# Optimization experiments

Hardware: AMD Instinct MI355X
Metric: run time of the kernel (lower is better)

Reference implementation:

```python
import jax, jax.numpy as jnp
import numpy as np

# dims (see shape_source)
BS, CIN, HF, WF = 4, 256, 56, 120   # packed batch, state channels, feature HxW (image/8)
CF, D = 64, 48                      # lifted feature channels, depth bins
DOWNSAMPLE = 8                      # image->feature stride (frustum in image pixels)
BEVX = BEVY = 128                   # BEV.SIZE // BEV.FEATURE_DOWNSAMPLE
SCALE = 0.6                         # BEV.RESOLUTION * BEV.FEATURE_DOWNSAMPLE (m/cell)
OFFX = 32.0                         # BEV.OFFSET_FORWARD / BEV.FEATURE_DOWNSAMPLE
D0, DSTEP = 2.0, 1.0                # dbound = [2.0, 50.0, 1.0]


def _conv(x, w, b, pad):
    y = jax.lax.conv_general_dilated(x, w, (1, 1), [(pad, pad), (pad, pad)],
                                     dimension_numbers=('NCHW', 'OIHW', 'NCHW'))
    return y + b[None, :, None, None]


def _block(x, w, b, g, bt, pad):
    # Conv2dBlock: conv -> BN (inference, running_mean=0 / running_var=1) -> relu
    y = _conv(x, w, b, pad)
    return jax.nn.relu(g[None, :, None, None] * y + bt[None, :, None, None])


def _forward(state, intr, extr, feat_w, feat_b, feat_g, feat_bt,
             dec_w, dec_b, dec_g, dec_bt, depth_w, depth_b):
    # image feature + depth distribution heads
    x = _block(state, feat_w, feat_b, feat_g, feat_bt, 2)           # [BS,CF,HF,WF]
    df = _block(state, dec_w, dec_b, dec_g, dec_bt, 2)              # [BS,CF,HF,WF]
    depth = jax.nn.softmax(_conv(df, depth_w, depth_b, 0), axis=1)  # [BS,D,HF,WF]

    # lift: outer product of depth distribution with features
    lift = depth[:, None, :, :, :] * x[:, :, None, :, :]            # [BS,CF,D,HF,WF]
    feats = lift.transpose(0, 2, 3, 4, 1)                           # [BS,D,HF,WF,CF]

    # frustum geometry: pixel (u,v,d) -> camera -> ego frame
    ds = D0 + jnp.arange(D, dtype=jnp.float32) * DSTEP              # [D]
    u = (jnp.arange(WF, dtype=jnp.float32) + 0.5) * DOWNSAMPLE      # image-pixel u
    v = (jnp.arange(HF, dtype=jnp.float32) + 0.5) * DOWNSAMPLE      # image-pixel v
    ud = u[None, None, :] * ds[:, None, None]                       # [D,1,WF] bcast
    vd = v[None, :, None] * ds[:, None, None]
    dd = jnp.broadcast_to(ds[:, None, None], (D, HF, WF))
    pix = jnp.stack(jnp.broadcast_arrays(ud, vd, dd), axis=-1)      # [D,HF,WF,3]
    Kinv = jnp.linalg.inv(intr)
    cam = pix @ Kinv.T                                              # camera frame
    R, t = extr[:3, :3], extr[:3, 3]
    ego = cam @ R.T + t                                             # [D,HF,WF,3]

    # voxelize into BEV grid + scatter-accumulate (splat)
    ix = jnp.floor(ego[..., 0] / SCALE + OFFX + BEVX / 2).astype(jnp.int32)
    iy = jnp.floor(ego[..., 1] / SCALE + BEVY / 2).astype(jnp.int32)
    valid = (ix >= 0) & (ix < BEVX) & (iy >= 0) & (iy < BEVY)       # [D,HF,WF]
    cell = iy * BEVX + ix
    batch_off = (jnp.arange(BS, dtype=jnp.int32) * (BEVY * BEVX))[:, None, None, None]
    seg = jnp.where(valid[None], batch_off + cell[None], BS * BEVY * BEVX)  # dump bin
    pooled = jax.ops.segment_sum(feats.reshape(BS * D * HF * WF, CF),
                                 seg.reshape(-1),
                                 num_segments=BS * BEVY * BEVX + 1)[:-1]
    bev = pooled.reshape(BS, BEVY, BEVX, CF).transpose(0, 3, 1, 2)  # [BS,CF,Y,X]
    return bev


def setup_inputs() -> dict:
    key = jax.random.key(0)
    ks = jax.random.split(key, 4)
    s = 0.02
    state = jax.random.normal(ks[0], (BS, CIN, HF, WF), jnp.float32)
    intr = jnp.array([[500., 0., 480.], [0., 500., 224.], [0., 0., 1.]], jnp.float32)
    # camera z -> ego x (forward), mounted at x=1.5m, z=2.0m
    extr = jnp.array([[0., 0., 1., 1.5], [-1., 0., 0., 0.],
                      [0., -1., 0., 2.0], [0., 0., 0., 1.]], jnp.float32)
    return {
        'state': state, 'intr': intr, 'extr': extr,
        'feat_w': jax.random.normal(ks[1], (CF, CIN, 5, 5), jnp.float32) * s,
        'feat_b': jnp.zeros((CF,), jnp.float32),
        'feat_g': jnp.ones((CF,), jnp.float32),
        'feat_bt': jnp.zeros((CF,), jnp.float32),
        'dec_w': jax.random.normal(ks[2], (CF, CIN, 5, 5), jnp.float32) * s,
        'dec_b': jnp.zeros((CF,), jnp.float32),
        'dec_g': jnp.ones((CF,), jnp.float32),
        'dec_bt': jnp.zeros((CF,), jnp.float32),
        'depth_w': jax.random.normal(ks[3], (D, CF, 1, 1), jnp.float32) * s,
        'depth_b': jnp.zeros((D,), jnp.float32),
    }


def reference(state, intr, extr, feat_w, feat_b, feat_g, feat_bt,
              dec_w, dec_b, dec_g, dec_bt, depth_w, depth_b):
    return _forward(state, intr, extr, feat_w, feat_b, feat_g, feat_bt,
                    dec_w, dec_b, dec_g, dec_bt, depth_w, depth_b)
```

## Files before the change

kernel.cpp:

```cpp
#include <hip/hip_runtime.h>
#include <hip/hip_bf16.h>
#include <math.h>

#define BS 4
#define CIN 256
#define HF 56
#define WF 120
#define CF 64
#define DD 48
#define HW (HF*WF)
#define BEVX 128
#define BEVY 128
#define NCELL (BEVX*BEVY)
#define NPTS (DD*HW)

#define PH 60
#define PW 124

#define PACKW_BLOCKS 400
#define CELL_BLOCKS  23

typedef short s16x8 __attribute__((ext_vector_type(8)));
typedef float f32x4 __attribute__((ext_vector_type(4)));

__device__ __forceinline__ unsigned short f2bf(float f) {
    unsigned int u = __float_as_uint(f);
    unsigned int r = (u + 0x7FFFu + ((u >> 16) & 1u)) >> 16;
    return (unsigned short)r;
}
__device__ __forceinline__ float bf2f(unsigned short s) {
    return __uint_as_float(((unsigned int)s) << 16);
}

__global__ __launch_bounds__(256) void pad_kernel(
    const float* __restrict__ state, unsigned short* __restrict__ P)
{
    __shared__ float lt[32 * 257];
    const int tile = blockIdx.x;
    const int b    = blockIdx.y;
    const int tid  = threadIdx.x;
    const int4 z4 = make_int4(0, 0, 0, 0);

    if (tile < 210) {
        const int hw0 = tile * 32;
        const int wl = tid & 31;
        const int cg = tid >> 5;
        const float* src = state + (size_t)(b * CIN + cg * 32) * HW + hw0 + wl;
#pragma unroll 8
        for (int k = 0; k < 32; ++k)
            lt[wl * 257 + cg * 32 + k] = src[(size_t)k * HW];
        __syncthreads();

        const int px = tid >> 3;
        const int ck = tid & 7;
        const int hw = hw0 + px;
        const int h = hw / WF, w = hw - h * WF;
        unsigned short* dst = P + (((size_t)b * PH + h + 2) * PW + (w + 2)) * CIN;
#pragma unroll
        for (int r = 0; r < 4; ++r) {
            const int c0 = r * 64 + ck * 8;
            unsigned short tmp[8];
#pragma unroll
            for (int j = 0; j < 8; ++j) tmp[j] = f2bf(lt[px * 257 + c0 + j]);
            *(int4*)(dst + c0) = *(const int4*)tmp;
        }
    } else {
        const int pxid = (tile - 210) * 32 + (tid >> 3);
        const int ck = tid & 7;
        if (pxid < 720) {
            int h2, w2;
            if (pxid < 496) { int r = pxid / 124; h2 = (r < 2) ? r : 56 + r; w2 = pxid - r * 124; }
            else { int u = pxid - 496; h2 = 2 + (u >> 2); int m = u & 3; w2 = (m < 2) ? m : 120 + m; }
            unsigned short* dst = P + (((size_t)b * PH + h2) * PW + w2) * CIN;
#pragma unroll
            for (int r = 0; r < 4; ++r)
                *(int4*)(dst + r * 64 + ck * 8) = z4;
        }
    }
}

__global__ __launch_bounds__(256) void prep_kernel(
    const float* __restrict__ intr, const float* __restrict__ extr,
    const float* __restrict__ fw, const float* __restrict__ dw,
    const float* __restrict__ fb, const float* __restrict__ fg, const float* __restrict__ fbt,
    const float* __restrict__ db, const float* __restrict__ dg, const float* __restrict__ dbt,
    const float* __restrict__ dpw,
    unsigned short* __restrict__ Wf, float2* __restrict__ aff,
    unsigned short* __restrict__ Wd, int* __restrict__ celltab)
{
    const int bid = blockIdx.x;
    const int tid = threadIdx.x;

    if (bid < PACKW_BLOCKS) {
        int t = bid * 256 + tid;
        int lane = t & 63;
        int nf = (t >> 6) & 7;
        int kc = (t >> 9) & 7;
        int p  = t >> 12;
        int n   = nf * 16 + (lane & 15);
        int ci0 = kc * 32 + (lane >> 4) * 8;
        const float* src = (n < 64) ? fw + (size_t)n * CIN * 25
                                    : dw + (size_t)(n - 64) * CIN * 25;
        unsigned short v[8];
#pragma unroll
        for (int j = 0; j < 8; ++j)
            v[j] = f2bf(src[(size_t)(ci0 + j) * 25 + p]);
        *(int4*)(Wf + (size_t)t * 8) = *(const int4*)v;
    } else if (bid == PACKW_BLOCKS) {
        if (tid < 128) {
            float g, bi, bt;
            if (tid < 64) { g = fg[tid]; bi = fb[tid]; bt = fbt[tid]; }
            else          { g = dg[tid - 64]; bi = db[tid - 64]; bt = dbt[tid - 64]; }
            aff[tid] = make_float2(g, g * bi + bt);
        }
        for (int e = tid; e < 384; e += 256) {
            int ln = e & 63;
            int s  = (e >> 6) & 1;
            int t  = e >> 7;
            unsigned short v[8];
#pragma unroll
            for (int j = 0; j < 8; ++j)
                v[j] = f2bf(dpw[(16 * t + (ln & 15)) * CF + s * 32 + (ln >> 4) * 8 + j]);
            *(int4*)(Wd + (size_t)e * 8) = *(const int4*)v;
        }
    } else {
        int pair = (bid - PACKW_BLOCKS - 1) * 256 + tid;
        if (pair >= DD * WF) return;
        int d = pair / WF;
        int w = pair - d * WF;
        int h = 0;

        float k00 = intr[0], k01 = intr[1], k02 = intr[2];
        float k11 = intr[4], k12 = intr[5];
        float k22 = intr[8];

        float A00 = __fdiv_rn(1.0f, k00);
        float A11 = __fdiv_rn(1.0f, k11);
        float A01 = __fmul_rn(__fmul_rn(k01, A00), -A11);
        float A22 = __fdiv_rn(1.0f, k22);
        float x0  = __fmul_rn(k02, A00);
        x0        = __fadd_rn(x0, __fmul_rn(k12, A01));
        float x1  = __fmul_rn(k12, A11);
        float A02 = __fmul_rn(x0, -A22);
        float A12 = __fmul_rn(x1, -A22);

        float i00 = A00, i01 = A01, i02 = A02;
        float i10 = 0.f, i11 = A11, i12 = A12;
        float i20 = 0.f, i21 = 0.f, i22 = A22;

        float u   = (w + 0.5f) * 8.0f;
        float v   = (h + 0.5f) * 8.0f;
        float dsv = 2.0f + (float)d;
        float px  = __fmul_rn(u, dsv);
        float py  = __fmul_rn(v, dsv);
        float pz  = dsv;

        float cam0 = fmaf(pz, i02, fmaf(py, i01, fmaf(px, i00, 0.0f)));
        float cam1 = fmaf(pz, i12, fmaf(py, i11, fmaf(px, i10, 0.0f)));
        float cam2 = fmaf(pz, i22, fmaf(py, i21, fmaf(px, i20, 0.0f)));

        float r00 = extr[0], r01 = extr[1], r02 = extr[2],  t0 = extr[3];
        float r10 = extr[4], r11 = extr[5], r12 = extr[6],  t1 = extr[7];

        float mm0 = fmaf(cam2, r02, fmaf(cam1, r01, fmaf(cam0, r00, 0.0f)));
        float mm1 = fmaf(cam2, r12, fmaf(cam1, r11, fmaf(cam0, r10, 0.0f)));
        float e0  = __fadd_rn(mm0, t0);
        float e1  = __fadd_rn(mm1, t1);

        float ixf = floorf(__fadd_rn(__fadd_rn(__fdiv_rn(e0, 0.6f), 32.0f), 64.0f));
        float iyf = floorf(__fadd_rn(__fdiv_rn(e1, 0.6f), 64.0f));
        int ix = (int)ixf;
        int iy = (int)iyf;

        bool valid = (ix >= 0) && (ix < BEVX) && (iy >= 0) && (iy < BEVY);
        celltab[pair] = valid ? iy * BEVX + ix : -1;
    }
}

__global__ __launch_bounds__(256) void conv_mfma_kernel(
    const unsigned short* __restrict__ P, const unsigned short* __restrict__ Wf,
    const float2* __restrict__ aff,
    unsigned short* __restrict__ xTb, unsigned short* __restrict__ decB)
{
    __shared__ __align__(16) unsigned short lds[2][144 * 32];

    const int tid  = threadIdx.x;
    const int lane = tid & 63;
    const int wid  = tid >> 6;
    const int wm   = wid >> 1;
    const int wn_g = ((blockIdx.z & 1) << 1) + (wid & 1);
    const int b  = blockIdx.z >> 1;
    const int h0 = blockIdx.y * 8;
    const int w0 = blockIdx.x * 8;

    const unsigned short* Pb = P + (((size_t)b * PH + h0) * PW + w0) * CIN;

    const int pix0 = tid >> 2,          slot0 = tid & 3;
    const size_t g0 = ((size_t)(pix0 / 12) * PW + (pix0 % 12)) * CIN + slot0 * 8;
    const int l0 = pix0 * 32 + (slot0 ^ ((pix0 >> 1) & 3)) * 8;
    const int c1 = 256 + tid;
    const int pix1 = c1 >> 2,           slot1 = c1 & 3;
    const size_t g1 = ((size_t)(pix1 / 12) * PW + (pix1 % 12)) * CIN + slot1 * 8;
    const int l1 = pix1 * 32 + (slot1 ^ ((pix1 >> 1) & 3)) * 8;
    const int c2 = 512 + tid;
    const int pix2 = c2 >> 2,           slot2 = c2 & 3;
    const size_t g2 = ((size_t)(pix2 / 12) * PW + (pix2 % 12)) * CIN + slot2 * 8;
    const int l2 = pix2 * 32 + (slot2 ^ ((pix2 >> 1) & 3)) * 8;
    const bool has3 = (tid < 64);

    f32x4 acc[2][2];
#pragma unroll
    for (int i = 0; i < 2; ++i)
#pragma unroll
        for (int j = 0; j < 2; ++j)
            acc[i][j] = (f32x4){0.f, 0.f, 0.f, 0.f};

    const int kg = lane >> 4;
    const int m0 = wm * 32 + (lane & 15);
    const int m1 = m0 + 16;
    const int pb0 = ((m0 >> 3)) * 12 + (m0 & 7);
    const int pb1 = ((m1 >> 3)) * 12 + (m1 & 7);

    {
        int4 r0 = *(const int4*)(Pb + g0);
        int4 r1 = *(const int4*)(Pb + g1);
        int4 r2;
        if (has3) r2 = *(const int4*)(Pb + g2);
        *(int4*)((char*)lds[0] + (size_t)l0 * 2) = r0;
        *(int4*)((char*)lds[0] + (size_t)l1 * 2) = r1;
        if (has3) *(int4*)((char*)lds[0] + (size_t)l2 * 2) = r2;
    }
    __syncthreads();

    for (int kc = 0; kc < 8; ++kc) {
        const int cur = kc & 1;
        int4 n0, n1, n2;
        if (kc < 7) {
            n0 = *(const int4*)(Pb + g0 + (size_t)(kc + 1) * 32);
            n1 = *(const int4*)(Pb + g1 + (size_t)(kc + 1) * 32);
            if (has3) n2 = *(const int4*)(Pb + g2 + (size_t)(kc + 1) * 32);
        }
        const unsigned short* lb = lds[cur];
#pragma unroll 5
        for (int p = 0; p < 25; ++p) {
            const int poff = (p / 5) * 12 + (p % 5);
            const int px0 = pb0 + poff;
            const int px1 = pb1 + poff;
            s16x8 a0 = *(const s16x8*)(lb + px0 * 32 + (kg ^ ((px0 >> 1) & 3)) * 8);
            s16x8 a1 = *(const s16x8*)(lb + px1 * 32 + (kg ^ ((px1 >> 1) & 3)) * 8);
            const size_t we = (((size_t)(p * 8 + kc) * 8) + wn_g * 2) * 64 + lane;
            s16x8 b0 = *(const s16x8*)(Wf + we * 8);
            s16x8 b1 = *(const s16x8*)(Wf + we * 8 + 512);
            acc[0][0] = __builtin_amdgcn_mfma_f32_16x16x32_bf16(a0, b0, acc[0][0], 0, 0, 0);
            acc[1][0] = __builtin_amdgcn_mfma_f32_16x16x32_bf16(a1, b0, acc[1][0], 0, 0, 0);
            acc[0][1] = __builtin_amdgcn_mfma_f32_16x16x32_bf16(a0, b1, acc[0][1], 0, 0, 0);
            acc[1][1] = __builtin_amdgcn_mfma_f32_16x16x32_bf16(a1, b1, acc[1][1], 0, 0, 0);
        }
        if (kc < 7) {
            *(int4*)((char*)lds[cur ^ 1] + (size_t)l0 * 2) = n0;
            *(int4*)((char*)lds[cur ^ 1] + (size_t)l1 * 2) = n1;
            if (has3) *(int4*)((char*)lds[cur ^ 1] + (size_t)l2 * 2) = n2;
        }
        __syncthreads();
    }

#pragma unroll
    for (int nf = 0; nf < 2; ++nf) {
        const int n = wn_g * 32 + nf * 16 + (lane & 15);
        const float2 sc = aff[n];
        unsigned short* dst = (n < 64) ? xTb : decB;
        const int ch = n & 63;
#pragma unroll
        for (int mf = 0; mf < 2; ++mf) {
#pragma unroll
            for (int r = 0; r < 4; ++r) {
                const int m = wm * 32 + mf * 16 + (lane >> 4) * 4 + r;
                const int h = h0 + (m >> 3), w = w0 + (m & 7);
                dst[(((size_t)b * HW) + h * WF + w) * 64 + ch] =
                    f2bf(fmaxf(sc.x * acc[mf][nf][r] + sc.y, 0.f));
            }
        }
    }
}

__global__ __launch_bounds__(256) void depth_kernel(
    const unsigned short* __restrict__ decB, const unsigned short* __restrict__ Wd,
    const float* __restrict__ dbs, float* __restrict__ depP, float4* __restrict__ poolz)
{
    {
        const int gid = blockIdx.x * 256 + threadIdx.x;
        const float4 z = make_float4(0.f, 0.f, 0.f, 0.f);
#pragma unroll
        for (int r = 0; r < 10; ++r) {
            int i = gid + r * (420 * 256);
            if (i < (BS * NCELL * CF) / 4) poolz[i] = z;
        }
    }

    const int lane = threadIdx.x & 63;
    const int wave = blockIdx.x * 4 + (threadIdx.x >> 6);
    const int px0  = wave * 16;

    const unsigned short* A = decB + (size_t)px0 * 64 + (lane & 15) * 64 + (lane >> 4) * 8;
    s16x8 a0 = *(const s16x8*)(A);
    s16x8 a1 = *(const s16x8*)(A + 32);

    f32x4 acc[3];
    float dbv[3];
#pragma unroll
    for (int t = 0; t < 3; ++t) {
        acc[t] = (f32x4){0.f, 0.f, 0.f, 0.f};
        dbv[t] = dbs[16 * t + (lane & 15)];
        s16x8 b0 = *(const s16x8*)(Wd + ((size_t)(t * 2 + 0) * 64 + lane) * 8);
        s16x8 b1 = *(const s16x8*)(Wd + ((size_t)(t * 2 + 1) * 64 + lane) * 8);
        acc[t] = __builtin_amdgcn_mfma_f32_16x16x32_bf16(a0, b0, acc[t], 0, 0, 0);
        acc[t] = __builtin_amdgcn_mfma_f32_16x16x32_bf16(a1, b1, acc[t], 0, 0, 0);
    }

#pragma unroll
    for (int r = 0; r < 4; ++r) {
        float l0 = acc[0][r] + dbv[0];
        float l1 = acc[1][r] + dbv[1];
        float l2 = acc[2][r] + dbv[2];
        float m = fmaxf(fmaxf(l0, l1), l2);
#pragma unroll
        for (int o = 1; o < 16; o <<= 1) m = fmaxf(m, __shfl_xor(m, o));
        float e0 = expf(l0 - m), e1 = expf(l1 - m), e2 = expf(l2 - m);
        float s = e0 + e1 + e2;
#pragma unroll
        for (int o = 1; o < 16; o <<= 1) s += __shfl_xor(s, o);
        float inv = 1.0f / s;
        float* op = depP + (size_t)(px0 + (lane >> 4) * 4 + r) * DD + (lane & 15);
        op[0]  = e0 * inv;
        op[16] = e1 * inv;
        op[32] = e2 * inv;
    }
}

__global__ __launch_bounds__(256) void colsum_kernel(
    const unsigned short* __restrict__ xTb, const float* __restrict__ depP,
    const int* __restrict__ celltab, float* __restrict__ pooled)
{
    const int w  = blockIdx.x;
    const int b  = blockIdx.z;
    const int lane = threadIdx.x & 63;
    const int wv   = threadIdx.x >> 6;
    const int dbase = blockIdx.y * 16 + wv * 4;

    int cells[4];
    bool anyv = false;
#pragma unroll
    for (int j = 0; j < 4; ++j) {
        cells[j] = celltab[(dbase + j) * WF + w];
        anyv |= (cells[j] >= 0);
    }
    if (!anyv) return;

    const unsigned short* xp = xTb + (((size_t)b * HW) + w) * 64 + lane;
    const float* dp = depP + (((size_t)b * HW) + w) * DD + dbase;

    float acc[4] = {0.f, 0.f, 0.f, 0.f};
#pragma unroll 8
    for (int h = 0; h < HF; ++h) {
        float xv = bf2f(xp[(size_t)h * WF * 64]);
        float4 dv = *(const float4*)(dp + (size_t)h * WF * DD);
        acc[0] = fmaf(dv.x, xv, acc[0]);
        acc[1] = fmaf(dv.y, xv, acc[1]);
        acc[2] = fmaf(dv.z, xv, acc[2]);
        acc[3] = fmaf(dv.w, xv, acc[3]);
    }

    float* pb = pooled + (size_t)b * NCELL * CF;
#pragma unroll
    for (int j = 0; j < 4; ++j)
        if (cells[j] >= 0)
            atomicAdd(&pb[(size_t)cells[j] * CF + lane], acc[j]);
}

__global__ __launch_bounds__(256) void transpose_kernel(
    const float* __restrict__ pooled, float* __restrict__ out)
{
    __shared__ float t[64][65];
    const int b  = blockIdx.y;
    const int c0 = blockIdx.x * 64;
    const int tid = threadIdx.x;
#pragma unroll
    for (int k = 0; k < 16; ++k) {
        int idx = tid + k * 256;
        int cell = idx >> 6, ch = idx & 63;
        t[cell][ch] = pooled[(((size_t)b * NCELL) + c0 + cell) * CF + ch];
    }
    __syncthreads();
#pragma unroll
    for (int k = 0; k < 16; ++k) {
        int idx = tid + k * 256;
        int ch = idx >> 6, cell = idx & 63;
        out[((size_t)b * CF + ch) * NCELL + c0 + cell] = t[cell][ch];
    }
}

extern "C" void kernel_launch(void* const* d_in, const int* in_sizes, int n_in,
                              void* d_out, int out_size, void* d_ws, size_t ws_size,
                              hipStream_t stream)
{
    const float* state   = (const float*)d_in[0];
    const float* intr    = (const float*)d_in[1];
    const float* extr    = (const float*)d_in[2];
    const float* feat_w  = (const float*)d_in[3];
    const float* feat_b  = (const float*)d_in[4];
    const float* feat_g  = (const float*)d_in[5];
    const float* feat_bt = (const float*)d_in[6];
    const float* dec_w   = (const float*)d_in[7];
    const float* dec_b   = (const float*)d_in[8];
    const float* dec_g   = (const float*)d_in[9];
    const float* dec_bt  = (const float*)d_in[10];
    const float* depth_w = (const float*)d_in[11];
    const float* depth_b = (const float*)d_in[12];
    float* out = (float*)d_out;

    char* ws = (char*)d_ws;
    const size_t P_BYTES   = (size_t)BS * PH * PW * CIN * 2;
    const size_t WF_BYTES  = (size_t)25 * 8 * 8 * 64 * 16;
    const size_t AFF_BYTES = 1024;
    const size_t WD_BYTES  = 384 * 16;
    const size_t FB_BYTES  = (size_t)BS * HW * CF * 2;
    const size_t DEP_BYTES = (size_t)BS * HW * DD * 4;
    const size_t CT_BYTES  = ((size_t)DD * WF + 64) * 4;

    unsigned short* P    = (unsigned short*)ws;           ws += P_BYTES;
    unsigned short* Wfr  = (unsigned short*)ws;           ws += WF_BYTES;
    float2*         aff  = (float2*)ws;                   ws += AFF_BYTES;
    unsigned short* Wd   = (unsigned short*)ws;           ws += WD_BYTES;
    unsigned short* xTb  = (unsigned short*)ws;           ws += FB_BYTES;
    unsigned short* decB = (unsigned short*)ws;           ws += FB_BYTES;
    float*          depP = (float*)ws;                    ws += DEP_BYTES;
    int*            celltab = (int*)ws;                   ws += CT_BYTES;

    float* pooled = (float*)d_ws;

    pad_kernel<<<dim3(233, BS), 256, 0, stream>>>(state, P);

    prep_kernel<<<PACKW_BLOCKS + 1 + CELL_BLOCKS, 256, 0, stream>>>(
        intr, extr, feat_w, dec_w,
        feat_b, feat_g, feat_bt, dec_b, dec_g, dec_bt, depth_w,
        Wfr, aff, Wd, celltab);

    conv_mfma_kernel<<<dim3(15, 7, BS * 2), 256, 0, stream>>>(
        P, Wfr, aff, xTb, decB);

    depth_kernel<<<420, 256, 0, stream>>>(decB, Wd, depth_b, depP, (float4*)pooled);

    colsum_kernel<<<dim3(WF, 3, BS), 256, 0, stream>>>(xTb, depP, celltab, pooled);

    transpose_kernel<<<dim3(NCELL / 64, BS), 256, 0, stream>>>(pooled, out);
}
```

Before: 189.7 us.

## Merge conv N-halves into one block and split taps across warp groups

The conv kernel now runs 512-thread blocks that each compute all 128 output channels (both feature and depth-decoder heads) for an 8x8 tile, instead of two blocks per tile each doing half the channels. The 25 filter taps are split between two groups of four waves, and the partial accumulators are reduced through shared memory before the epilogue. This halves redundant input-tile loads into LDS and keeps the same wave count per tile. In exchange it adds a 32KB LDS reduction buffer, an extra barrier, more accumulator registers per wave, and an uneven 13/12 tap split, which may lower occupancy.

```diff
diff --git a/kernel.cpp b/kernel.cpp
--- a/kernel.cpp
+++ b/kernel.cpp
@@ -177,19 +177,44 @@
     }
 }
 
-__global__ __launch_bounds__(256) void conv_mfma_kernel(
+#define CONV_TAPS(PL, PH_)                                                              \
+    for (int p = PL; p < PH_; ++p) {                                                    \
+        const int poff = (p / 5) * 12 + (p % 5);                                        \
+        const int px0 = pb0 + poff;                                                     \
+        const int px1 = pb1 + poff;                                                     \
+        s16x8 a0 = *(const s16x8*)(lb + px0 * 32 + (kg ^ ((px0 >> 1) & 3)) * 8);        \
+        s16x8 a1 = *(const s16x8*)(lb + px1 * 32 + (kg ^ ((px1 >> 1) & 3)) * 8);        \
+        const unsigned short* wp =                                                      \
+            Wf + ((((size_t)(p * 8 + kc)) * 8 + wn * 4) * 64 + lane) * 8;               \
+        s16x8 b0 = *(const s16x8*)(wp);                                                 \
+        s16x8 b1 = *(const s16x8*)(wp + 512);                                           \
+        s16x8 b2 = *(const s16x8*)(wp + 1024);                                          \
+        s16x8 b3 = *(const s16x8*)(wp + 1536);                                          \
+        acc[0][0] = __builtin_amdgcn_mfma_f32_16x16x32_bf16(a0, b0, acc[0][0], 0, 0, 0);\
+        acc[1][0] = __builtin_amdgcn_mfma_f32_16x16x32_bf16(a1, b0, acc[1][0], 0, 0, 0);\
+        acc[0][1] = __builtin_amdgcn_mfma_f32_16x16x32_bf16(a0, b1, acc[0][1], 0, 0, 0);\
+        acc[1][1] = __builtin_amdgcn_mfma_f32_16x16x32_bf16(a1, b1, acc[1][1], 0, 0, 0);\
+        acc[0][2] = __builtin_amdgcn_mfma_f32_16x16x32_bf16(a0, b2, acc[0][2], 0, 0, 0);\
+        acc[1][2] = __builtin_amdgcn_mfma_f32_16x16x32_bf16(a1, b2, acc[1][2], 0, 0, 0);\
+        acc[0][3] = __builtin_amdgcn_mfma_f32_16x16x32_bf16(a0, b3, acc[0][3], 0, 0, 0);\
+        acc[1][3] = __builtin_amdgcn_mfma_f32_16x16x32_bf16(a1, b3, acc[1][3], 0, 0, 0);\
+    }
+
+__global__ __launch_bounds__(512) void conv_mfma_kernel(
     const unsigned short* __restrict__ P, const unsigned short* __restrict__ Wf,
     const float2* __restrict__ aff,
     unsigned short* __restrict__ xTb, unsigned short* __restrict__ decB)
 {
     __shared__ __align__(16) unsigned short lds[2][144 * 32];
+    __shared__ __align__(16) float red[4 * 8 * 64 * 4];
 
     const int tid  = threadIdx.x;
     const int lane = tid & 63;
     const int wid  = tid >> 6;
-    const int wm   = wid >> 1;
-    const int wn_g = ((blockIdx.z & 1) << 1) + (wid & 1);
-    const int b  = blockIdx.z >> 1;
+    const int tp   = wid >> 2;
+    const int wn   = (wid >> 1) & 1;
+    const int wm   = wid & 1;
+    const int b  = blockIdx.z;
     const int h0 = blockIdx.y * 8;
     const int w0 = blockIdx.x * 8;
 
@@ -198,21 +223,17 @@
     const int pix0 = tid >> 2,          slot0 = tid & 3;
     const size_t g0 = ((size_t)(pix0 / 12) * PW + (pix0 % 12)) * CIN + slot0 * 8;
     const int l0 = pix0 * 32 + (slot0 ^ ((pix0 >> 1) & 3)) * 8;
-    const int c1 = 256 + tid;
+    const int c1 = 512 + tid;
     const int pix1 = c1 >> 2,           slot1 = c1 & 3;
     const size_t g1 = ((size_t)(pix1 / 12) * PW + (pix1 % 12)) * CIN + slot1 * 8;
     const int l1 = pix1 * 32 + (slot1 ^ ((pix1 >> 1) & 3)) * 8;
-    const int c2 = 512 + tid;
-    const int pix2 = c2 >> 2,           slot2 = c2 & 3;
-    const size_t g2 = ((size_t)(pix2 / 12) * PW + (pix2 % 12)) * CIN + slot2 * 8;
-    const int l2 = pix2 * 32 + (slot2 ^ ((pix2 >> 1) & 3)) * 8;
-    const bool has3 = (tid < 64);
-
-    f32x4 acc[2][2];
+    const bool has2 = (tid < 64);
+
+    f32x4 acc[2][4];
 #pragma unroll
     for (int i = 0; i < 2; ++i)
 #pragma unroll
-        for (int j = 0; j < 2; ++j)
+        for (int j = 0; j < 4; ++j)
             acc[i][j] = (f32x4){0.f, 0.f, 0.f, 0.f};
 
     const int kg = lane >> 4;
@@ -223,50 +244,51 @@
 
     {
         int4 r0 = *(const int4*)(Pb + g0);
-        int4 r1 = *(const int4*)(Pb + g1);
-        int4 r2;
-        if (has3) r2 = *(const int4*)(Pb + g2);
+        int4 r1;
+        if (has2) r1 = *(const int4*)(Pb + g1);
         *(int4*)((char*)lds[0] + (size_t)l0 * 2) = r0;
-        *(int4*)((char*)lds[0] + (size_t)l1 * 2) = r1;
-        if (has3) *(int4*)((char*)lds[0] + (size_t)l2 * 2) = r2;
+        if (has2) *(int4*)((char*)lds[0] + (size_t)l1 * 2) = r1;
     }
     __syncthreads();
 
     for (int kc = 0; kc < 8; ++kc) {
         const int cur = kc & 1;
-        int4 n0, n1, n2;
+        int4 n0, n1;
         if (kc < 7) {
             n0 = *(const int4*)(Pb + g0 + (size_t)(kc + 1) * 32);
-            n1 = *(const int4*)(Pb + g1 + (size_t)(kc + 1) * 32);
-            if (has3) n2 = *(const int4*)(Pb + g2 + (size_t)(kc + 1) * 32);
+            if (has2) n1 = *(const int4*)(Pb + g1 + (size_t)(kc + 1) * 32);
         }
         const unsigned short* lb = lds[cur];
-#pragma unroll 5
-        for (int p = 0; p < 25; ++p) {
-            const int poff = (p / 5) * 12 + (p % 5);
-            const int px0 = pb0 + poff;
-            const int px1 = pb1 + poff;
-            s16x8 a0 = *(const s16x8*)(lb + px0 * 32 + (kg ^ ((px0 >> 1) & 3)) * 8);
-            s16x8 a1 = *(const s16x8*)(lb + px1 * 32 + (kg ^ ((px1 >> 1) & 3)) * 8);
-            const size_t we = (((size_t)(p * 8 + kc) * 8) + wn_g * 2) * 64 + lane;
-            s16x8 b0 = *(const s16x8*)(Wf + we * 8);
-            s16x8 b1 = *(const s16x8*)(Wf + we * 8 + 512);
-            acc[0][0] = __builtin_amdgcn_mfma_f32_16x16x32_bf16(a0, b0, acc[0][0], 0, 0, 0);
-            acc[1][0] = __builtin_amdgcn_mfma_f32_16x16x32_bf16(a1, b0, acc[1][0], 0, 0, 0);
-            acc[0][1] = __builtin_amdgcn_mfma_f32_16x16x32_bf16(a0, b1, acc[0][1], 0, 0, 0);
-            acc[1][1] = __builtin_amdgcn_mfma_f32_16x16x32_bf16(a1, b1, acc[1][1], 0, 0, 0);
-        }
+        if (tp == 0) { CONV_TAPS(0, 13) } else { CONV_TAPS(13, 25) }
         if (kc < 7) {
             *(int4*)((char*)lds[cur ^ 1] + (size_t)l0 * 2) = n0;
-            *(int4*)((char*)lds[cur ^ 1] + (size_t)l1 * 2) = n1;
-            if (has3) *(int4*)((char*)lds[cur ^ 1] + (size_t)l2 * 2) = n2;
+            if (has2) *(int4*)((char*)lds[cur ^ 1] + (size_t)l1 * 2) = n1;
         }
         __syncthreads();
     }
 
-#pragma unroll
-    for (int nf = 0; nf < 2; ++nf) {
-        const int n = wn_g * 32 + nf * 16 + (lane & 15);
+    const int pair = wm * 2 + wn;
+    if (tp == 1) {
+#pragma unroll
+        for (int mf = 0; mf < 2; ++mf)
+#pragma unroll
+            for (int nf = 0; nf < 4; ++nf)
+                *(f32x4*)&red[((pair * 8 + mf * 4 + nf) * 64 + lane) * 4] = acc[mf][nf];
+    }
+    __syncthreads();
+    if (tp == 1) return;
+
+#pragma unroll
+    for (int mf = 0; mf < 2; ++mf)
+#pragma unroll
+        for (int nf = 0; nf < 4; ++nf) {
+            f32x4 o = *(const f32x4*)&red[((pair * 8 + mf * 4 + nf) * 64 + lane) * 4];
+            acc[mf][nf] += o;
+        }
+
+#pragma unroll
+    for (int nf = 0; nf < 4; ++nf) {
+        const int n = wn * 64 + nf * 16 + (lane & 15);
         const float2 sc = aff[n];
         unsigned short* dst = (n < 64) ? xTb : decB;
         const int ch = n & 63;
@@ -445,7 +467,7 @@
         feat_b, feat_g, feat_bt, dec_b, dec_g, dec_bt, depth_w,
         Wfr, aff, Wd, celltab);
 
-    conv_mfma_kernel<<<dim3(15, 7, BS * 2), 256, 0, stream>>>(
+    conv_mfma_kernel<<<dim3(15, 7, BS), 512, 0, stream>>>(
         P, Wfr, aff, xTb, decB);
 
     depth_kernel<<<420, 256, 0, stream>>>(decB, Wd, depth_b, depP, (float4*)pooled);
```

After: 285.7 us. +50.6%, slower.
